# Kernel tuning notes

Measured on AMD Instinct MI355X. Metric: run time of the kernel, lower is better.

## Reference

```python
import jax, jax.numpy as jnp
import numpy as np

T = 64
LAMBDA_SCALE = 4
RECON = 512
U = 2 ** (LAMBDA_SCALE - 1)          # 8
YT = RECON // U                      # 64
P = YT * YT                          # 4096


def convert_Ht2Weights(Ht, u):
    # Ht: [T, recon, recon] -> per-low-res-pixel weights [P, T, u*u]
    t, r, _ = Ht.shape
    yt = r // u
    w = Ht.reshape(t, yt, u, yt, u)
    w = jnp.transpose(w, (1, 3, 0, 2, 4))        # [yt, yt, T, u, u]
    return w.reshape(yt * yt, t, u * u)


def setup_inputs() -> dict:
    key = jax.random.key(0)
    k1, k2, k3 = jax.random.split(key, 3)
    yt = jax.random.normal(k1, (64, T, YT, YT), dtype=jnp.float32)
    Ht = jax.random.normal(k2, (T, RECON, RECON), dtype=jnp.float32)
    biases = jax.random.normal(k3, (P, 1, U * U), dtype=jnp.float32)
    return {"yt": yt, "Ht": Ht, "biases": biases}


def reference(yt, Ht, biases):
    B = yt.shape[0]
    # [B, T, yt, yt] -> [P, B, T]
    y = yt.reshape(B, T, P).transpose(2, 0, 1)
    weights = convert_Ht2Weights(Ht, U)          # [P, T, u*u]
    # per-pixel batched GEMM + bias
    up = jnp.einsum('pbt,ptu->pbu', y, weights) + biases   # [P, B, u*u]
    # pixel-shuffle back to full resolution
    up = up.reshape(YT, YT, B, U, U)
    up = jnp.transpose(up, (2, 0, 3, 1, 4)).reshape(B, RECON, RECON)
    return up[:, None]                            # [B, 1, recon, recon] (seq_block = identity)
```

## Files before the change

kernel.cpp:

```cpp
#include <hip/hip_runtime.h>

typedef float f32x4 __attribute__((ext_vector_type(4)));
typedef short s16x8 __attribute__((ext_vector_type(8)));
typedef unsigned int u32;

__device__ __forceinline__ u32 f2bf(float x) {
    u32 u = __float_as_uint(x);
    return (u + 0x7FFFu + ((u >> 16) & 1u)) >> 16;
}
__device__ __forceinline__ u32 pk(float a, float b) {
    return f2bf(a) | (f2bf(b) << 16);
}
__device__ __forceinline__ int swz(int row, int t) {
    int g = ((row ^ (row >> 3)) & 7) << 3;
    return row * 64 + (t ^ g);
}

__global__ __launch_bounds__(512, 4)
void upsample_mfma_kernel(const float* __restrict__ yt,
                          const float* __restrict__ Ht,
                          const float* __restrict__ biases,
                          float* __restrict__ out)
{
    __shared__ __align__(16) unsigned short S[32768];

    const int wg  = blockIdx.x;
    const int py  = (wg & 7) + ((wg >> 3) & 7) * 8;
    const int pxo = wg >> 6;
    const int px0 = pxo * 8;
    const int tid = (int)threadIdx.x;

    {
        const int c4 = tid & 15;
        const int uy = (tid >> 4) & 7;
        const int tq = tid >> 7;
        const float* wb = Ht + (size_t)(py * 8 + uy) * 512 + px0 * 8 + c4 * 4;
        #pragma unroll
        for (int ph = 0; ph < 2; ++ph) {
            const int t0 = ph * 32 + tq * 8;
            f32x4 v[8];
            #pragma unroll
            for (int k = 0; k < 8; ++k)
                v[k] = *(const f32x4*)(wb + (size_t)(t0 + k) * 262144);
            #pragma unroll
            for (int cc = 0; cc < 4; ++cc) {
                const int c   = c4 * 4 + cc;
                const int pxl = c >> 3;
                const int uu  = uy * 8 + (c & 7);
                uint4 g;
                g.x = pk(v[0][cc], v[1][cc]);
                g.y = pk(v[2][cc], v[3][cc]);
                g.z = pk(v[4][cc], v[5][cc]);
                g.w = pk(v[6][cc], v[7][cc]);
                *(uint4*)&S[pxl * 4096 + swz(uu, t0)] = g;
            }
        }
    }
    __syncthreads();

    const int wv = tid >> 6;
    const int l = tid & 63, r = l & 15, q = l >> 4;
    s16x8 wf[4][2];
    #pragma unroll
    for (int nb = 0; nb < 4; ++nb)
        #pragma unroll
        for (int ks = 0; ks < 2; ++ks)
            wf[nb][ks] = *(const s16x8*)&S[wv * 4096 + swz(nb * 16 + r, ks * 32 + q * 8)];

    const int px = px0 + wv;
    const int p  = py * 64 + px;
    float bv[4];
    #pragma unroll
    for (int nb = 0; nb < 4; ++nb)
        bv[nb] = biases[(size_t)p * 64 + nb * 16 + r];

    __syncthreads();

    {
        const int pxh = tid & 1;
        const int ab  = (tid >> 1) & 31;
        const int atq = tid >> 6;
        const float* abase = yt + (size_t)py * 64 + px0 + pxh * 4
                           + (size_t)atq * 8 * 4096;
        #pragma unroll
        for (int bc = 0; bc < 2; ++bc) {
            const float* ap = abase + (size_t)(bc * 32 + ab) * 262144;
            f32x4 v[8];
            #pragma unroll
            for (int k = 0; k < 8; ++k)
                v[k] = *(const f32x4*)(ap + (size_t)k * 4096);
            #pragma unroll
            for (int i = 0; i < 4; ++i) {
                uint4 g;
                g.x = pk(v[0][i], v[1][i]);
                g.y = pk(v[2][i], v[3][i]);
                g.z = pk(v[4][i], v[5][i]);
                g.w = pk(v[6][i], v[7][i]);
                *(uint4*)&S[bc * 16384 + (pxh * 4 + i) * 2048 + swz(ab, atq * 8)] = g;
            }
        }
    }
    __syncthreads();

    #pragma unroll
    for (int bc = 0; bc < 2; ++bc) {
        f32x4 acc[2][4];
        #pragma unroll
        for (int mb = 0; mb < 2; ++mb)
            #pragma unroll
            for (int nb = 0; nb < 4; ++nb)
                acc[mb][nb] = (f32x4){bv[nb], bv[nb], bv[nb], bv[nb]};

        #pragma unroll
        for (int ks = 0; ks < 2; ++ks) {
            s16x8 af[2];
            #pragma unroll
            for (int mb = 0; mb < 2; ++mb)
                af[mb] = *(const s16x8*)&S[bc * 16384 + wv * 2048
                                           + swz(mb * 16 + r, ks * 32 + q * 8)];
            #pragma unroll
            for (int mb = 0; mb < 2; ++mb)
                #pragma unroll
                for (int nb = 0; nb < 4; ++nb)
                    acc[mb][nb] = __builtin_amdgcn_mfma_f32_16x16x32_bf16(
                        af[mb], wf[nb][ks], acc[mb][nb], 0, 0, 0);
        }

        #pragma unroll
        for (int mb = 0; mb < 2; ++mb) {
            #pragma unroll
            for (int nb = 0; nb < 4; ++nb) {
                const int n   = nb * 16 + r;
                const int row = py * 8 + (n >> 3);
                const int col = px * 8 + (n & 7);
                float* ob = out + ((size_t)(bc * 32 + mb * 16 + q * 4) * 512 + row) * 512 + col;
                #pragma unroll
                for (int ii = 0; ii < 4; ++ii)
                    ob[(size_t)ii * 262144] = acc[mb][nb][ii];
            }
        }
    }
}

extern "C" void kernel_launch(void* const* d_in, const int* in_sizes, int n_in,
                              void* d_out, int out_size, void* d_ws, size_t ws_size,
                              hipStream_t stream) {
    const float* yt     = (const float*)d_in[0];
    const float* Ht     = (const float*)d_in[1];
    const float* biases = (const float*)d_in[2];
    float* out          = (float*)d_out;
    upsample_mfma_kernel<<<dim3(512), dim3(512), 0, stream>>>(yt, Ht, biases, out);
}
```

Before: 39.99 us.

## Pipeline activation loads in batch chunks and stage output through LDS for coalesced stores

Splits the batch into four 16-sample chunks with a double-buffered LDS slot, prefetching the next chunk's activations into registers while the current chunk's MFMAs run. The first activation load is issued before the weight staging to hide its latency. Results are bounced through a swizzled LDS region so each output row segment is written with 16-byte coalesced stores instead of scattered 4-byte stores. The block-to-row mapping is also changed so consecutive workgroups on one XCD share rows. This costs extra __syncthreads per chunk and more LDS traffic.

```diff
diff --git a/kernel.cpp b/kernel.cpp
--- a/kernel.cpp
+++ b/kernel.cpp
@@ -15,6 +15,16 @@
     int g = ((row ^ (row >> 3)) & 7) << 3;
     return row * 64 + (t ^ g);
 }
+__device__ __forceinline__ int swzA(int row, int t) {
+    return row * 64 + (t ^ ((row & 7) << 3));
+}
+__device__ __forceinline__ int bh(int rowid) {
+    return (rowid ^ (rowid >> 4)) & 15;
+}
+
+#define A_PLANE 1032
+#define A_SLOT  (8 * A_PLANE)
+#define BOUNCE  (2 * A_SLOT)
 
 __global__ __launch_bounds__(512, 4)
 void upsample_mfma_kernel(const float* __restrict__ yt,
@@ -22,123 +32,132 @@
                           const float* __restrict__ biases,
                           float* __restrict__ out)
 {
-    __shared__ __align__(16) unsigned short S[32768];
+    __shared__ __align__(16) unsigned short S[32896];
 
     const int wg  = blockIdx.x;
-    const int py  = (wg & 7) + ((wg >> 3) & 7) * 8;
-    const int pxo = wg >> 6;
+    const int xcd = wg & 7;
+    const int j   = wg >> 3;
+    const int py  = xcd * 8 + (j & 7);
+    const int pxo = j >> 3;
     const int px0 = pxo * 8;
     const int tid = (int)threadIdx.x;
 
+    const int pxh = tid & 1;
+    const int ab  = (tid >> 1) & 15;
+    const int atq = tid >> 5;
+    const float* a_base = yt + (size_t)ab * 262144 + (size_t)atq * 4 * 4096
+                        + py * 64 + px0 + pxh * 4;
+
+    f32x4 v[4];
+    #pragma unroll
+    for (int k = 0; k < 4; ++k)
+        v[k] = *(const f32x4*)(a_base + (size_t)k * 4096);
+
     {
-        const int c4 = tid & 15;
-        const int uy = (tid >> 4) & 7;
-        const int tq = tid >> 7;
+        const int c4 = tid & 15, uy = (tid >> 4) & 7, tq = tid >> 7;
         const float* wb = Ht + (size_t)(py * 8 + uy) * 512 + px0 * 8 + c4 * 4;
         #pragma unroll
         for (int ph = 0; ph < 2; ++ph) {
             const int t0 = ph * 32 + tq * 8;
-            f32x4 v[8];
+            f32x4 w8[8];
             #pragma unroll
             for (int k = 0; k < 8; ++k)
-                v[k] = *(const f32x4*)(wb + (size_t)(t0 + k) * 262144);
+                w8[k] = *(const f32x4*)(wb + (size_t)(t0 + k) * 262144);
             #pragma unroll
             for (int cc = 0; cc < 4; ++cc) {
-                const int c   = c4 * 4 + cc;
-                const int pxl = c >> 3;
-                const int uu  = uy * 8 + (c & 7);
+                const int c = c4 * 4 + cc, pxl = c >> 3, uu = uy * 8 + (c & 7);
                 uint4 g;
-                g.x = pk(v[0][cc], v[1][cc]);
-                g.y = pk(v[2][cc], v[3][cc]);
-                g.z = pk(v[4][cc], v[5][cc]);
-                g.w = pk(v[6][cc], v[7][cc]);
+                g.x = pk(w8[0][cc], w8[1][cc]);
+                g.y = pk(w8[2][cc], w8[3][cc]);
+                g.z = pk(w8[4][cc], w8[5][cc]);
+                g.w = pk(w8[6][cc], w8[7][cc]);
                 *(uint4*)&S[pxl * 4096 + swz(uu, t0)] = g;
             }
         }
     }
     __syncthreads();
 
-    const int wv = tid >> 6;
-    const int l = tid & 63, r = l & 15, q = l >> 4;
+    const int wv = tid >> 6, l = tid & 63, r = l & 15, q = l >> 4;
     s16x8 wf[4][2];
     #pragma unroll
     for (int nb = 0; nb < 4; ++nb)
         #pragma unroll
         for (int ks = 0; ks < 2; ++ks)
             wf[nb][ks] = *(const s16x8*)&S[wv * 4096 + swz(nb * 16 + r, ks * 32 + q * 8)];
-
-    const int px = px0 + wv;
-    const int p  = py * 64 + px;
+    const int px = px0 + wv, p = py * 64 + px;
     float bv[4];
     #pragma unroll
     for (int nb = 0; nb < 4; ++nb)
         bv[nb] = biases[(size_t)p * 64 + nb * 16 + r];
-
     __syncthreads();
 
-    {
-        const int pxh = tid & 1;
-        const int ab  = (tid >> 1) & 31;
-        const int atq = tid >> 6;
-        const float* abase = yt + (size_t)py * 64 + px0 + pxh * 4
-                           + (size_t)atq * 8 * 4096;
+    auto writeA = [&](int slot) {
         #pragma unroll
-        for (int bc = 0; bc < 2; ++bc) {
-            const float* ap = abase + (size_t)(bc * 32 + ab) * 262144;
-            f32x4 v[8];
-            #pragma unroll
-            for (int k = 0; k < 8; ++k)
-                v[k] = *(const f32x4*)(ap + (size_t)k * 4096);
-            #pragma unroll
-            for (int i = 0; i < 4; ++i) {
-                uint4 g;
-                g.x = pk(v[0][i], v[1][i]);
-                g.y = pk(v[2][i], v[3][i]);
-                g.z = pk(v[4][i], v[5][i]);
-                g.w = pk(v[6][i], v[7][i]);
-                *(uint4*)&S[bc * 16384 + (pxh * 4 + i) * 2048 + swz(ab, atq * 8)] = g;
-            }
+        for (int pp = 0; pp < 4; ++pp) {
+            const int pxl = pxh * 4 + pp;
+            *(uint2*)&S[slot * A_SLOT + pxl * A_PLANE + swzA(ab, atq * 4)] =
+                make_uint2(pk(v[0][pp], v[1][pp]), pk(v[2][pp], v[3][pp]));
         }
-    }
+    };
+    auto issueA = [&](int chunk) {
+        const float* ap = a_base + (size_t)chunk * 16 * 262144;
+        #pragma unroll
+        for (int k = 0; k < 4; ++k)
+            v[k] = *(const f32x4*)(ap + (size_t)k * 4096);
+    };
+
+    writeA(0);
+    issueA(1);
     __syncthreads();
 
+    float* Sf = (float*)&S[BOUNCE];
+
     #pragma unroll
-    for (int bc = 0; bc < 2; ++bc) {
-        f32x4 acc[2][4];
+    for (int i = 0; i < 4; ++i) {
+        f32x4 acc[4];
         #pragma unroll
-        for (int mb = 0; mb < 2; ++mb)
+        for (int nb = 0; nb < 4; ++nb)
+            acc[nb] = (f32x4){bv[nb], bv[nb], bv[nb], bv[nb]};
+        #pragma unroll
+        for (int ks = 0; ks < 2; ++ks) {
+            s16x8 af = *(const s16x8*)&S[(i & 1) * A_SLOT + wv * A_PLANE
+                                         + swzA(r, ks * 32 + q * 8)];
             #pragma unroll
             for (int nb = 0; nb < 4; ++nb)
-                acc[mb][nb] = (f32x4){bv[nb], bv[nb], bv[nb], bv[nb]};
+                acc[nb] = __builtin_amdgcn_mfma_f32_16x16x32_bf16(
+                    af, wf[nb][ks], acc[nb], 0, 0, 0);
+        }
 
-        #pragma unroll
-        for (int ks = 0; ks < 2; ++ks) {
-            s16x8 af[2];
-            #pragma unroll
-            for (int mb = 0; mb < 2; ++mb)
-                af[mb] = *(const s16x8*)&S[bc * 16384 + wv * 2048
-                                           + swz(mb * 16 + r, ks * 32 + q * 8)];
-            #pragma unroll
-            for (int mb = 0; mb < 2; ++mb)
-                #pragma unroll
-                for (int nb = 0; nb < 4; ++nb)
-                    acc[mb][nb] = __builtin_amdgcn_mfma_f32_16x16x32_bf16(
-                        af[mb], wf[nb][ks], acc[mb][nb], 0, 0, 0);
+        if (i < 3) {
+            writeA((i + 1) & 1);
+            if (i < 2) issueA(i + 2);
         }
 
         #pragma unroll
-        for (int mb = 0; mb < 2; ++mb) {
+        for (int nb = 0; nb < 4; ++nb) {
+            const int uy  = nb * 2 + (r >> 3);
+            const int c4l = wv * 2 + ((r & 7) >> 2);
+            const int e   = r & 3;
             #pragma unroll
-            for (int nb = 0; nb < 4; ++nb) {
-                const int n   = nb * 16 + r;
-                const int row = py * 8 + (n >> 3);
-                const int col = px * 8 + (n & 7);
-                float* ob = out + ((size_t)(bc * 32 + mb * 16 + q * 4) * 512 + row) * 512 + col;
-                #pragma unroll
-                for (int ii = 0; ii < 4; ++ii)
-                    ob[(size_t)ii * 262144] = acc[mb][nb][ii];
+            for (int ii = 0; ii < 4; ++ii) {
+                const int bl    = q * 4 + ii;
+                const int rowid = bl * 8 + uy;
+                Sf[rowid * 64 + ((c4l ^ bh(rowid)) << 2) + e] = acc[nb][ii];
             }
         }
+        __syncthreads();
+
+        #pragma unroll
+        for (int jj = 0; jj < 4; ++jj) {
+            const int slot = jj * 512 + tid;
+            const int bl = slot >> 7, rem = slot & 127;
+            const int uy = rem >> 4, c4 = rem & 15;
+            const int rowid = bl * 8 + uy;
+            f32x4 vv = *(const f32x4*)&Sf[rowid * 64 + ((c4 ^ bh(rowid)) << 2)];
+            *(f32x4*)&out[((size_t)(i * 16 + bl) * 512 + py * 8 + uy) * 512
+                          + px0 * 8 + c4 * 4] = vv;
+        }
+        __syncthreads();
     }
 }
 
```

Result: faster. 36.75 us, median of 2 (-8.1%).
